# Performance work log

Measured on AMD Instinct MI355X. Metric: run time of the kernel, lower is better.

## Reference

```python
import jax, jax.numpy as jnp
import numpy as np

B, LC, LR, D, H = 32, 2048, 512, 256, 128  # D = 2*hidden_size, fc maps 4*D -> H


def setup_inputs() -> dict:
    key = jax.random.key(0)
    k1, k2, k3, k4 = jax.random.split(key, 4)
    scale = 1.0 / np.sqrt(D)
    return {
        "context_input": jax.random.normal(k1, (B, LC, D), dtype=jnp.float32),
        "response_input": jax.random.normal(k2, (B, LR, D), dtype=jnp.float32),
        "W1": jax.random.normal(k3, (H, 4 * D), dtype=jnp.float32) * scale,
        "b1": jnp.zeros((H,), dtype=jnp.float32),
        "W2": jax.random.normal(k4, (H, 4 * D), dtype=jnp.float32) * scale,
        "b2": jnp.zeros((H,), dtype=jnp.float32),
    }


def reference(context_input, response_input, W1, b1, W2, b2):
    cs = context_input   # [B, Lc, D]
    rs = response_input  # [B, Lr, D]
    # shared score matrix, reused by both softmaxes
    e = jnp.einsum("bcd,brd->bcr", cs, rs)          # [B, Lc, Lr]
    alpha = jax.nn.softmax(e, axis=2)                 # over response positions
    beta = jax.nn.softmax(e, axis=1)                  # over context positions
    cd = jnp.einsum("bcr,brd->bcd", alpha, rs)       # [B, Lc, D]
    rd = jnp.einsum("bcr,bcd->brd", beta, cs)        # [B, Lr, D]
    raw_cl = jnp.concatenate((cs, cd, cs - cd, cs * cd), axis=2)  # [B, Lc, 4D]
    raw_rl = jnp.concatenate((rs, rd, rs - rd, rs * rd), axis=2)  # [B, Lr, 4D]
    # dropout is identity in eval mode
    cl = jax.nn.relu(jnp.einsum("bcf,hf->bch", raw_cl, W1) + b1)  # [B, Lc, H]
    rl = jax.nn.relu(jnp.einsum("brf,hf->brh", raw_rl, W2) + b2)  # [B, Lr, H]
    return (cl, rl)
```

## Files before the change

kernel.cpp:

```cpp
#include <hip/hip_runtime.h>


#define NB  32
#define NLC 2048
#define NLR 512
#define ND  256
#define NH  128

typedef float f32x4 __attribute__((ext_vector_type(4)));
typedef short s16x8 __attribute__((ext_vector_type(8)));
typedef short s16x4 __attribute__((ext_vector_type(4)));

#define WS_CSH 0ull
#define WS_CSL (WS_CSH + 33554432ull)
#define WS_RSH (WS_CSL + 33554432ull)
#define WS_RSL (WS_RSH + 8388608ull)
#define WS_RST (WS_RSL + 8388608ull)
#define WS_CST (WS_RST + 8388608ull)
#define WS_WH  (WS_CST + 33554432ull)
#define WS_NEED (WS_WH + 524288ull)

#define BUFSZ 49152
#define SM_P  98304
#define SM_O  0

__device__ __forceinline__ unsigned short f2bf(float x){
  unsigned u = __builtin_bit_cast(unsigned, x);
  u += 0x7FFFu + ((u >> 16) & 1u);
  return (unsigned short)(u >> 16);
}
__device__ __forceinline__ float bf2f(unsigned short h){
  unsigned u = ((unsigned)h) << 16;
  return __builtin_bit_cast(float, u);
}
__device__ __forceinline__ void splitbf(float x, short &hi, short &lo){
  unsigned short h = f2bf(x);
  float r = x - bf2f(h);
  hi = (short)h;
  lo = (short)f2bf(r);
}
__device__ __forceinline__ void gll16(const void* g, void* l){
  __builtin_amdgcn_global_load_lds((const __attribute__((address_space(1))) void*)g,
                                   (__attribute__((address_space(3))) void*)l, 16, 0, 0);
}


__global__ __launch_bounds__(256)
void prep_rows(const float* __restrict__ cs, const float* __restrict__ rs,
               const float* __restrict__ W1, const float* __restrict__ W2,
               unsigned char* __restrict__ ws)
{
  const int tid = threadIdx.x, lane = tid & 63, wid = tid >> 6;
  const int bid = blockIdx.x;
  if (bid < 20480){
    const float* srcrow; unsigned char *dsth, *dstl; int kvl;
    if (bid < 16384){
      int row = bid*4 + wid;
      int b = row >> 11, pos = row & 2047, t = pos >> 5; kvl = pos & 31;
      srcrow = cs + (size_t)row*ND;
      size_t off = ((size_t)(b*64 + t)*32 + kvl)*512;
      dsth = ws + WS_CSH + off; dstl = ws + WS_CSL + off;
    } else {
      int row = (bid - 16384)*4 + wid;
      int b = row >> 9, pos = row & 511, t = pos >> 5; kvl = pos & 31;
      srcrow = rs + (size_t)row*ND;
      size_t off = ((size_t)(b*16 + t)*32 + kvl)*512;
      dsth = ws + WS_RSH + off; dstl = ws + WS_RSL + off;
    }
    float4 x = *((const float4*)srcrow + lane);
    short h0,l0,h1,l1,h2,l2,h3,l3;
    splitbf(x.x,h0,l0); splitbf(x.y,h1,l1); splitbf(x.z,h2,l2); splitbf(x.w,h3,l3);
    int boff = (8*lane) ^ ((kvl & 7) << 4);
    *(s16x4*)(dsth + boff) = (s16x4){h0,h1,h2,h3};
    *(s16x4*)(dstl + boff) = (s16x4){l0,l1,l2,l3};
  } else {
    int idx = (bid - 20480)*2048 + tid*8;
    const float* srcw = (idx < 131072) ? (W1 + idx) : (W2 + (idx - 131072));
    float4 a = *(const float4*)srcw;
    float4 c4 = *((const float4*)srcw + 1);
    s16x8 h;
    h[0]=(short)f2bf(a.x); h[1]=(short)f2bf(a.y); h[2]=(short)f2bf(a.z); h[3]=(short)f2bf(a.w);
    h[4]=(short)f2bf(c4.x); h[5]=(short)f2bf(c4.y); h[6]=(short)f2bf(c4.z); h[7]=(short)f2bf(c4.w);
    *(s16x8*)(ws + WS_WH + (size_t)idx*2) = h;
  }
}

__global__ __launch_bounds__(256)
void prep_T(const float* __restrict__ cs, const float* __restrict__ rs,
            unsigned char* __restrict__ ws)
{
  __shared__ float tile[32][256];
  const int tid = threadIdx.x, lane = tid & 63, wid = tid >> 6;
  const int bid = blockIdx.x;
  const float* src; unsigned char* dst;
  if (bid < 512){ int b = bid >> 4, t = bid & 15;
    src = rs + ((size_t)b*NLR + t*32)*ND;
    dst = ws + WS_RST + (size_t)bid*16384;
  } else { int b2 = bid - 512; int b = b2 >> 6, t = b2 & 63;
    src = cs + ((size_t)b*NLC + t*32)*ND;
    dst = ws + WS_CST + (size_t)b2*16384;
  }
  #pragma unroll
  for (int i = 0; i < 8; ++i){
    int r = wid*8 + i;
    float4 x = *((const float4*)(src + (size_t)r*ND) + lane);
    *(float4*)&tile[r][lane*4] = x;
  }
  __syncthreads();
  const int d = tid;
  const int swzc = (d >> 2) & 3;
  unsigned char* orow = dst + d*64;
  #pragma unroll
  for (int ci = 0; ci < 4; ++ci){
    int sg = ci ^ swzc;
    s16x8 w;
    #pragma unroll
    for (int j = 0; j < 8; ++j){
      int kvl = 4*sg + (j >> 1) + ((j & 1) << 4);
      w[j] = (short)f2bf(tile[kvl][d]);
    }
    *(s16x8*)(orow + 16*ci) = w;
  }
}


__global__ __launch_bounds__(512, 2)
void lm_main(const unsigned char* __restrict__ ws,
             const float* __restrict__ b1, const float* __restrict__ b2,
             float* __restrict__ out)
{
  __shared__ __align__(16) char smem[106496];

  const int tid  = threadIdx.x;
  const int lane = tid & 63;
  const int wid  = tid >> 6;
  const int c    = lane & 15;
  const int g    = lane >> 4;

  int bid = blockIdx.x;
  int dir, b, qt;
  if (bid < 128){ dir = 1; int xcd = bid & 7, inner = bid >> 3;
    b = xcd*4 + (inner >> 2); qt = inner & 3; }
  else { dir = 0; int t2 = bid - 128; int xcd = t2 & 7, inner = t2 >> 3;
    b = xcd*4 + (inner >> 4); qt = inner & 15; }

  const unsigned char *QH, *QL, *KH, *KL, *VT;
  int NT;
  if (dir == 0){
    QH = ws + WS_CSH + (size_t)b*64*16384;  QL = ws + WS_CSL + (size_t)b*64*16384;
    KH = ws + WS_RSH + (size_t)b*16*16384;  KL = ws + WS_RSL + (size_t)b*16*16384;
    VT = ws + WS_RST + (size_t)b*16*16384;  NT = 16;
  } else {
    QH = ws + WS_RSH + (size_t)b*16*16384;  QL = ws + WS_RSL + (size_t)b*16*16384;
    KH = ws + WS_CSH + (size_t)b*64*16384;  KL = ws + WS_CSL + (size_t)b*64*16384;
    VT = ws + WS_CST + (size_t)b*64*16384;  NT = 64;
  }
  const unsigned char* Wp = ws + WS_WH + (size_t)dir*262144;
  const float* bia = dir ? b2 : b1;
  float* outp = dir == 0 ? out + ((size_t)b*NLC + qt*128)*NH
                         : out + (size_t)NB*NLC*NH + ((size_t)b*NLR + qt*128)*NH;

  s16x8 qh[8], ql[8];
  {
    int q = qt*128 + 16*wid + c;
    const unsigned char* qrowH = QH + (size_t)(q >> 5)*16384 + (size_t)(q & 31)*512;
    const unsigned char* qrowL = QL + (size_t)(q >> 5)*16384 + (size_t)(q & 31)*512;
    int qx = (q & 7) << 4;
    #pragma unroll
    for (int ks = 0; ks < 8; ++ks){
      int off = (64*ks + 16*g) ^ qx;
      qh[ks] = *(const s16x8*)(qrowH + off);
      ql[ks] = *(const s16x8*)(qrowL + off);
    }
  }

  f32x4 o[16];
  #pragma unroll
  for (int i = 0; i < 16; ++i) o[i] = (f32x4){0.f,0.f,0.f,0.f};
  float m_run[4] = {-INFINITY,-INFINITY,-INFINITY,-INFINITY};
  float l_run[4] = {0.f,0.f,0.f,0.f};

  #define STAGE(tt, bsel) do {                                              \
    const unsigned char* kh_ = KH + (size_t)(tt)*16384;                     \
    const unsigned char* kl_ = KL + (size_t)(tt)*16384;                     \
    const unsigned char* vt_ = VT + (size_t)(tt)*16384;                     \
    char* bb_ = smem + (bsel)*BUFSZ;                                        \
    _Pragma("unroll")                                                       \
    for (int i_ = 0; i_ < 6; ++i_){                                         \
      int j_ = 8*i_ + wid;                                                  \
      const unsigned char* src_; int dst_;                                  \
      if (j_ < 16){ src_ = kh_ + (size_t)j_*1024;        dst_ = j_*1024; }  \
      else if (j_ < 32){ src_ = kl_ + (size_t)(j_-16)*1024; dst_ = 16384 + (j_-16)*1024; } \
      else { src_ = vt_ + (size_t)(j_-32)*1024;          dst_ = 32768 + (j_-32)*1024; } \
      gll16(src_ + (size_t)lane*16, bb_ + dst_);                            \
    }                                                                       \
  } while(0)

  STAGE(0, 0);
  __syncthreads();
  int cur = 0;

  for (int t = 0; t < NT; ++t){
    if (t + 1 < NT) STAGE(t + 1, cur ^ 1);

    const char* B = smem + cur*BUFSZ;

    f32x4 s0 = (f32x4){0.f,0.f,0.f,0.f}, s1 = (f32x4){0.f,0.f,0.f,0.f};
    __builtin_amdgcn_s_setprio(1);
    #pragma unroll
    for (int ks = 0; ks < 8; ++ks){
      int kb = 64*ks + 16*g;
      int o0 = c*512 + (kb ^ ((c & 7) << 4));
      int o1 = (16 + c)*512 + (kb ^ (((16 + c) & 7) << 4));
      s16x8 bh0 = *(const s16x8*)(B + o0);
      s16x8 bl0 = *(const s16x8*)(B + 16384 + o0);
      s16x8 bh1 = *(const s16x8*)(B + o1);
      s16x8 bl1 = *(const s16x8*)(B + 16384 + o1);
      s0 = __builtin_amdgcn_mfma_f32_16x16x32_bf16(qh[ks], bh0, s0, 0,0,0);
      s1 = __builtin_amdgcn_mfma_f32_16x16x32_bf16(qh[ks], bh1, s1, 0,0,0);
      s0 = __builtin_amdgcn_mfma_f32_16x16x32_bf16(ql[ks], bh0, s0, 0,0,0);
      s1 = __builtin_amdgcn_mfma_f32_16x16x32_bf16(ql[ks], bh1, s1, 0,0,0);
      s0 = __builtin_amdgcn_mfma_f32_16x16x32_bf16(qh[ks], bl0, s0, 0,0,0);
      s1 = __builtin_amdgcn_mfma_f32_16x16x32_bf16(qh[ks], bl1, s1, 0,0,0);
    }
    __builtin_amdgcn_s_setprio(0);

    float scl[4];
    #pragma unroll
    for (int r = 0; r < 4; ++r){
      float v = fmaxf(s0[r], s1[r]);
      v = fmaxf(v, __shfl_xor(v, 1)); v = fmaxf(v, __shfl_xor(v, 2));
      v = fmaxf(v, __shfl_xor(v, 4)); v = fmaxf(v, __shfl_xor(v, 8));
      float mo = m_run[r];
      float mn = fmaxf(mo, v);
      m_run[r] = mn;
      float sc = __expf(mo - mn);
      scl[r] = sc;
      float p0 = __expf(s0[r] - mn);
      float p1 = __expf(s1[r] - mn);
      float ps = p0 + p1;
      ps += __shfl_xor(ps, 1); ps += __shfl_xor(ps, 2);
      ps += __shfl_xor(ps, 4); ps += __shfl_xor(ps, 8);
      l_run[r] = l_run[r]*sc + ps;
      int qr = 16*wid + 4*g + r;
      unsigned pk = (unsigned)f2bf(p0) | ((unsigned)f2bf(p1) << 16);
      *(unsigned*)(smem + SM_P + qr*64 + ((4*c) ^ (r << 4))) = pk;
    }
    #pragma unroll
    for (int dt = 0; dt < 16; ++dt){
      o[dt][0] *= scl[0]; o[dt][1] *= scl[1]; o[dt][2] *= scl[2]; o[dt][3] *= scl[3];
    }

    {
      int q2 = 16*wid + c;
      s16x8 pa = *(const s16x8*)(smem + SM_P + q2*64 + ((16*g) ^ ((q2 & 3) << 4)));
      __builtin_amdgcn_s_setprio(1);
      #pragma unroll
      for (int dt = 0; dt < 16; ++dt){
        int vrow = 16*dt + c;
        s16x8 vb = *(const s16x8*)(B + 32768 + vrow*64 + ((16*g) ^ (((vrow >> 2) & 3) << 4)));
        o[dt] = __builtin_amdgcn_mfma_f32_16x16x32_bf16(pa, vb, o[dt], 0,0,0);
      }
      __builtin_amdgcn_s_setprio(0);
    }

    __syncthreads();
    cur ^= 1;
  }

  {
    float inv[4];
    #pragma unroll
    for (int r = 0; r < 4; ++r) inv[r] = 1.0f / l_run[r];
    #pragma unroll
    for (int dt = 0; dt < 16; ++dt){
      #pragma unroll
      for (int r = 0; r < 4; ++r){
        int qr = 16*wid + 4*g + r;
        int dcol = 16*dt + c;
        float val = o[dt][r] * inv[r];
        *(short*)(smem + SM_O + qr*512 + ((2*dcol) ^ ((qr & 7) << 4))) = (short)f2bf(val);
      }
    }
  }

  f32x4 fa[8];
  #pragma unroll
  for (int i = 0; i < 8; ++i) fa[i] = (f32x4){0.f,0.f,0.f,0.f};

  #pragma unroll
  for (int fc = 0; fc < 8; ++fc){
    #pragma unroll
    for (int ksl = 0; ksl < 4; ++ksl){
      const int cidx = (fc & 1)*4 + ksl;
      s16x8 a;
      if (fc < 2){
        a = qh[cidx];
      } else {
        int q2 = 16*wid + c;
        s16x8 o8 = *(const s16x8*)(smem + SM_O + q2*512 + ((64*cidx + 16*g) ^ ((q2 & 7) << 4)));
        if (fc < 4){ a = o8; }
        else {
          #pragma unroll
          for (int j = 0; j < 8; ++j){
            float qf = bf2f((unsigned short)qh[cidx][j]) + bf2f((unsigned short)ql[cidx][j]);
            float of = bf2f((unsigned short)o8[j]);
            float fv = (fc < 6) ? (qf - of) : (qf * of);
            a[j] = (short)f2bf(fv);
          }
        }
      }
      #pragma unroll
      for (int nt = 0; nt < 8; ++nt){
        s16x8 wb = *(const s16x8*)(Wp + (size_t)(16*nt + c)*2048 + 2*(fc*128 + 32*ksl + 8*g));
        fa[nt] = __builtin_amdgcn_mfma_f32_16x16x32_bf16(a, wb, fa[nt], 0,0,0);
      }
    }
  }

  #pragma unroll
  for (int nt = 0; nt < 8; ++nt){
    float bs = bia[16*nt + c];
    #pragma unroll
    for (int r = 0; r < 4; ++r){
      int qr = 16*wid + 4*g + r;
      float v = fa[nt][r] + bs;
      v = fmaxf(v, 0.f);
      outp[(size_t)qr*NH + 16*nt + c] = v;
    }
  }
}


__global__ __launch_bounds__(256, 2)
void lm_fallback(const float* __restrict__ cs, const float* __restrict__ rs,
                 const float* __restrict__ W1, const float* __restrict__ b1,
                 const float* __restrict__ W2, const float* __restrict__ b2,
                 float* __restrict__ out)
{
  __shared__ __align__(16) char smem[65536];
  const int tid  = threadIdx.x;
  const int lane = tid & 63;
  const int wid  = tid >> 6;
  const int c    = lane & 15;
  const int g    = lane >> 4;

  int bid = blockIdx.x;
  int dir, b, qt;
  if (bid < 1024){ int xcd = bid & 7, inner = bid >> 3;
    b = (xcd << 2) + (inner >> 5); qt = inner & 31; dir = 0; }
  else { int t2 = bid - 1024; int xcd = t2 & 7, inner = t2 >> 3;
    b = (xcd << 2) + (inner >> 3); qt = inner & 7; dir = 1; }

  const float* Q   = dir == 0 ? cs + ((size_t)b*NLC + qt*64)*ND
                              : rs + ((size_t)b*NLR + qt*64)*ND;
  const float* KV  = dir == 0 ? rs + (size_t)b*NLR*ND : cs + (size_t)b*NLC*ND;
  const int    NK  = dir == 0 ? NLR : NLC;
  const float* Wm  = dir == 0 ? W1 : W2;
  const float* bia = dir == 0 ? b1 : b2;
  float* outp = dir == 0 ? out + ((size_t)b*NLC + qt*64)*NH
                         : out + (size_t)NB*NLC*NH + ((size_t)b*NLR + qt*64)*NH;

  s16x8 qh[8], ql[8];
  {
    const float* qrow = Q + (size_t)(16*wid + c)*ND;
    #pragma unroll
    for (int ks = 0; ks < 8; ++ks){
      float4 x0 = *(const float4*)(qrow + 32*ks + 8*g);
      float4 x1 = *(const float4*)(qrow + 32*ks + 8*g + 4);
      float xs[8] = {x0.x,x0.y,x0.z,x0.w,x1.x,x1.y,x1.z,x1.w};
      #pragma unroll
      for (int j = 0; j < 8; ++j){ short h,l; splitbf(xs[j],h,l); qh[ks][j]=h; ql[ks][j]=l; }
    }
  }

  f32x4 o[16];
  #pragma unroll
  for (int i = 0; i < 16; ++i) o[i] = (f32x4){0.f,0.f,0.f,0.f};
  float m_run[4] = {-INFINITY,-INFINITY,-INFINITY,-INFINITY};
  float l_run[4] = {0.f,0.f,0.f,0.f};

  const int ntile = NK >> 5;
  for (int t = 0; t < ntile; ++t){
    __syncthreads();
    {
      const float* KVt = KV + (size_t)t*32*ND;
      #pragma unroll
      for (int p = 0; p < 8; ++p){
        int kvloc = p*4 + wid;
        float4 x = *((const float4*)(KVt + kvloc*ND) + lane);
        short h0,l0,h1,l1,h2,l2,h3,l3;
        splitbf(x.x,h0,l0); splitbf(x.y,h1,l1); splitbf(x.z,h2,l2); splitbf(x.w,h3,l3);
        int roff = kvloc*512 + ((8*lane) ^ ((kvloc&7)<<4));
        *(s16x4*)(smem + 0     + roff) = (s16x4){h0,h1,h2,h3};
        *(s16x4*)(smem + 16384 + roff) = (s16x4){l0,l1,l2,l3};
        int d0 = 4*lane;
        short hs[4] = {h0,h1,h2,h3};
        #pragma unroll
        for (int j = 0; j < 4; ++j){
          int dr = d0 + j;
          int voff = dr*64 + ((2*kvloc) ^ (((dr>>2)&3)<<4));
          *(short*)(smem + 32768 + voff) = hs[j];
        }
      }
    }
    __syncthreads();

    f32x4 s0 = (f32x4){0.f,0.f,0.f,0.f}, s1 = (f32x4){0.f,0.f,0.f,0.f};
    #pragma unroll
    for (int ks = 0; ks < 8; ++ks){
      int kb = 64*ks + 16*g;
      int o0 = c*512 + (kb ^ ((c&7)<<4));
      int o1 = (16+c)*512 + (kb ^ (((16+c)&7)<<4));
      s16x8 bh0 = *(const s16x8*)(smem + 0     + o0);
      s16x8 bl0 = *(const s16x8*)(smem + 16384 + o0);
      s16x8 bh1 = *(const s16x8*)(smem + 0     + o1);
      s16x8 bl1 = *(const s16x8*)(smem + 16384 + o1);
      s0 = __builtin_amdgcn_mfma_f32_16x16x32_bf16(qh[ks], bh0, s0, 0,0,0);
      s1 = __builtin_amdgcn_mfma_f32_16x16x32_bf16(qh[ks], bh1, s1, 0,0,0);
      s0 = __builtin_amdgcn_mfma_f32_16x16x32_bf16(ql[ks], bh0, s0, 0,0,0);
      s1 = __builtin_amdgcn_mfma_f32_16x16x32_bf16(ql[ks], bh1, s1, 0,0,0);
      s0 = __builtin_amdgcn_mfma_f32_16x16x32_bf16(qh[ks], bl0, s0, 0,0,0);
      s1 = __builtin_amdgcn_mfma_f32_16x16x32_bf16(qh[ks], bl1, s1, 0,0,0);
    }

    float scl[4];
    #pragma unroll
    for (int r = 0; r < 4; ++r){
      float v = fmaxf(s0[r], s1[r]);
      v = fmaxf(v, __shfl_xor(v, 1)); v = fmaxf(v, __shfl_xor(v, 2));
      v = fmaxf(v, __shfl_xor(v, 4)); v = fmaxf(v, __shfl_xor(v, 8));
      float mo = m_run[r];
      float mn = fmaxf(mo, v);
      m_run[r] = mn;
      float sc = __expf(mo - mn);
      scl[r] = sc;
      float p0 = __expf(s0[r] - mn);
      float p1 = __expf(s1[r] - mn);
      float ps = p0 + p1;
      ps += __shfl_xor(ps, 1); ps += __shfl_xor(ps, 2);
      ps += __shfl_xor(ps, 4); ps += __shfl_xor(ps, 8);
      l_run[r] = l_run[r]*sc + ps;
      int q = 16*wid + 4*g + r;
      int pb = q*64;
      *(short*)(smem + 49152 + pb + (( 2*c     ) ^ (r<<4))) = (short)f2bf(p0);
      *(short*)(smem + 49152 + pb + ((32 + 2*c ) ^ (r<<4))) = (short)f2bf(p1);
    }
    #pragma unroll
    for (int dt = 0; dt < 16; ++dt){
      o[dt][0] *= scl[0]; o[dt][1] *= scl[1]; o[dt][2] *= scl[2]; o[dt][3] *= scl[3];
    }

    {
      int q = 16*wid + c;
      s16x8 pa = *(const s16x8*)(smem + 49152 + q*64 + ((16*g) ^ ((q&3)<<4)));
      #pragma unroll
      for (int dt = 0; dt < 16; ++dt){
        int vrow = 16*dt + c;
        s16x8 vb = *(const s16x8*)(smem + 32768 + vrow*64 + ((16*g) ^ (((vrow>>2)&3)<<4)));
        o[dt] = __builtin_amdgcn_mfma_f32_16x16x32_bf16(pa, vb, o[dt], 0,0,0);
      }
    }
  }

  __syncthreads();
  {
    float inv[4];
    #pragma unroll
    for (int r = 0; r < 4; ++r) inv[r] = 1.0f / l_run[r];
    #pragma unroll
    for (int dt = 0; dt < 16; ++dt){
      #pragma unroll
      for (int r = 0; r < 4; ++r){
        int q = 16*wid + 4*g + r;
        int dcol = 16*dt + c;
        float val = o[dt][r] * inv[r];
        *(short*)(smem + 0 + q*512 + ((2*dcol) ^ ((q&7)<<4))) = (short)f2bf(val);
      }
    }
  }

  f32x4 fa[8];
  #pragma unroll
  for (int i = 0; i < 8; ++i) fa[i] = (f32x4){0.f,0.f,0.f,0.f};

  #pragma unroll
  for (int fc = 0; fc < 8; ++fc){
    __syncthreads();
    #pragma unroll
    for (int p = 0; p < 8; ++p){
      int h  = p*16 + (tid >> 4);
      int fl = (tid & 15) * 8;
      const float* srcw = Wm + (size_t)h*1024 + fc*128 + fl;
      float4 x0 = *(const float4*)srcw;
      float4 x1 = *(const float4*)(srcw + 4);
      s16x8 w8;
      w8[0]=(short)f2bf(x0.x); w8[1]=(short)f2bf(x0.y); w8[2]=(short)f2bf(x0.z); w8[3]=(short)f2bf(x0.w);
      w8[4]=(short)f2bf(x1.x); w8[5]=(short)f2bf(x1.y); w8[6]=(short)f2bf(x1.z); w8[7]=(short)f2bf(x1.w);
      *(s16x8*)(smem + 32768 + h*256 + ((2*fl) ^ ((h&7)<<4))) = w8;
    }
    __syncthreads();
    #pragma unroll
    for (int ks = 0; ks < 4; ++ks){
      const int cidx = (fc & 1)*4 + ks;
      s16x8 a;
      if (fc < 2){
        a = qh[cidx];
      } else {
        int q = 16*wid + c;
        s16x8 o8 = *(const s16x8*)(smem + 0 + q*512 + ((64*cidx + 16*g) ^ ((q&7)<<4)));
        if (fc < 4){ a = o8; }
        else {
          #pragma unroll
          for (int j = 0; j < 8; ++j){
            float qf = bf2f((unsigned short)qh[cidx][j]) + bf2f((unsigned short)ql[cidx][j]);
            float of = bf2f((unsigned short)o8[j]);
            float fv = (fc < 6) ? (qf - of) : (qf * of);
            a[j] = (short)f2bf(fv);
          }
        }
      }
      #pragma unroll
      for (int nt = 0; nt < 8; ++nt){
        int hh = 16*nt + c;
        s16x8 wb = *(const s16x8*)(smem + 32768 + hh*256 + ((64*ks + 16*g) ^ ((hh&7)<<4)));
        fa[nt] = __builtin_amdgcn_mfma_f32_16x16x32_bf16(a, wb, fa[nt], 0,0,0);
      }
    }
  }

  #pragma unroll
  for (int nt = 0; nt < 8; ++nt){
    float bs = bia[16*nt + c];
    #pragma unroll
    for (int r = 0; r < 4; ++r){
      int q = 16*wid + 4*g + r;
      float v = fa[nt][r] + bs;
      v = fmaxf(v, 0.f);
      outp[(size_t)q*NH + 16*nt + c] = v;
    }
  }
}

extern "C" void kernel_launch(void* const* d_in, const int* in_sizes, int n_in,
                              void* d_out, int out_size, void* d_ws, size_t ws_size,
                              hipStream_t stream) {
  (void)in_sizes; (void)n_in; (void)out_size;
  const float* cs = (const float*)d_in[0];
  const float* rs = (const float*)d_in[1];
  const float* W1 = (const float*)d_in[2];
  const float* b1 = (const float*)d_in[3];
  const float* W2 = (const float*)d_in[4];
  const float* b2 = (const float*)d_in[5];
  float* out = (float*)d_out;

  if (ws_size >= WS_NEED){
    unsigned char* ws = (unsigned char*)d_ws;
    hipLaunchKernelGGL(prep_rows, dim3(20608), dim3(256), 0, stream, cs, rs, W1, W2, ws);
    hipLaunchKernelGGL(prep_T,    dim3(2560),  dim3(256), 0, stream, cs, rs, ws);
    hipLaunchKernelGGL(lm_main,   dim3(640),   dim3(512), 0, stream, ws, b1, b2, out);
  } else {
    hipLaunchKernelGGL(lm_fallback, dim3(1280), dim3(256), 0, stream,
                       cs, rs, W1, b1, W2, b2, out);
  }
}
```

Before: 484.3 us.

## Transpose score MFMA so softmax stays in registers, dropping P staging through LDS

Swaps the MFMA operand order so each lane holds one query's scores across key positions. The row max and sum now need only two cross-lane shuffles, and the probability fragment is packed directly into the B operand of the PV MFMA instead of round-tripping through shared memory. The V-transpose pack order is changed to match the new operand layout. Score accumulation is split into two interleaved accumulators to shorten MFMA dependency chains. This shrinks LDS use, adds one barrier before the epilogue, and relies on the reworked layout being consistent across the prep and main kernels.

```diff
diff --git a/kernel.cpp b/kernel.cpp
--- a/kernel.cpp
+++ b/kernel.cpp
@@ -10,6 +10,7 @@
 typedef float f32x4 __attribute__((ext_vector_type(4)));
 typedef short s16x8 __attribute__((ext_vector_type(8)));
 typedef short s16x4 __attribute__((ext_vector_type(4)));
+typedef int   i32x4 __attribute__((ext_vector_type(4)));
 
 #define WS_CSH 0ull
 #define WS_CSL (WS_CSH + 33554432ull)
@@ -21,7 +22,6 @@
 #define WS_NEED (WS_WH + 524288ull)
 
 #define BUFSZ 49152
-#define SM_P  98304
 #define SM_O  0
 
 __device__ __forceinline__ unsigned short f2bf(float x){
@@ -116,7 +116,7 @@
     s16x8 w;
     #pragma unroll
     for (int j = 0; j < 8; ++j){
-      int kvl = 4*sg + (j >> 1) + ((j & 1) << 4);
+      int kvl = 4*sg + (j & 3) + 16*((j >> 2) & 1);
       w[j] = (short)f2bf(tile[kvl][d]);
     }
     *(s16x8*)(orow + 16*ci) = w;
@@ -129,7 +129,7 @@
              const float* __restrict__ b1, const float* __restrict__ b2,
              float* __restrict__ out)
 {
-  __shared__ __align__(16) char smem[106496];
+  __shared__ __align__(16) char smem[98304];
 
   const int tid  = threadIdx.x;
   const int lane = tid & 63;
@@ -177,8 +177,8 @@
   f32x4 o[16];
   #pragma unroll
   for (int i = 0; i < 16; ++i) o[i] = (f32x4){0.f,0.f,0.f,0.f};
-  float m_run[4] = {-INFINITY,-INFINITY,-INFINITY,-INFINITY};
-  float l_run[4] = {0.f,0.f,0.f,0.f};
+  float m_run = -INFINITY;
+  float l_run = 0.f;
 
   #define STAGE(tt, bsel) do {                                              \
     const unsigned char* kh_ = KH + (size_t)(tt)*16384;                     \
@@ -205,7 +205,8 @@
 
     const char* B = smem + cur*BUFSZ;
 
-    f32x4 s0 = (f32x4){0.f,0.f,0.f,0.f}, s1 = (f32x4){0.f,0.f,0.f,0.f};
+    f32x4 s0a = (f32x4){0.f,0.f,0.f,0.f}, s0b = (f32x4){0.f,0.f,0.f,0.f};
+    f32x4 s1a = (f32x4){0.f,0.f,0.f,0.f}, s1b = (f32x4){0.f,0.f,0.f,0.f};
     __builtin_amdgcn_s_setprio(1);
     #pragma unroll
     for (int ks = 0; ks < 8; ++ks){
@@ -216,73 +217,79 @@
       s16x8 bl0 = *(const s16x8*)(B + 16384 + o0);
       s16x8 bh1 = *(const s16x8*)(B + o1);
       s16x8 bl1 = *(const s16x8*)(B + 16384 + o1);
-      s0 = __builtin_amdgcn_mfma_f32_16x16x32_bf16(qh[ks], bh0, s0, 0,0,0);
-      s1 = __builtin_amdgcn_mfma_f32_16x16x32_bf16(qh[ks], bh1, s1, 0,0,0);
-      s0 = __builtin_amdgcn_mfma_f32_16x16x32_bf16(ql[ks], bh0, s0, 0,0,0);
-      s1 = __builtin_amdgcn_mfma_f32_16x16x32_bf16(ql[ks], bh1, s1, 0,0,0);
-      s0 = __builtin_amdgcn_mfma_f32_16x16x32_bf16(qh[ks], bl0, s0, 0,0,0);
-      s1 = __builtin_amdgcn_mfma_f32_16x16x32_bf16(qh[ks], bl1, s1, 0,0,0);
+      if (ks & 1){
+        s0b = __builtin_amdgcn_mfma_f32_16x16x32_bf16(bh0, qh[ks], s0b, 0,0,0);
+        s1b = __builtin_amdgcn_mfma_f32_16x16x32_bf16(bh1, qh[ks], s1b, 0,0,0);
+        s0b = __builtin_amdgcn_mfma_f32_16x16x32_bf16(bh0, ql[ks], s0b, 0,0,0);
+        s1b = __builtin_amdgcn_mfma_f32_16x16x32_bf16(bh1, ql[ks], s1b, 0,0,0);
+        s0b = __builtin_amdgcn_mfma_f32_16x16x32_bf16(bl0, qh[ks], s0b, 0,0,0);
+        s1b = __builtin_amdgcn_mfma_f32_16x16x32_bf16(bl1, qh[ks], s1b, 0,0,0);
+      } else {
+        s0a = __builtin_amdgcn_mfma_f32_16x16x32_bf16(bh0, qh[ks], s0a, 0,0,0);
+        s1a = __builtin_amdgcn_mfma_f32_16x16x32_bf16(bh1, qh[ks], s1a, 0,0,0);
+        s0a = __builtin_amdgcn_mfma_f32_16x16x32_bf16(bh0, ql[ks], s0a, 0,0,0);
+        s1a = __builtin_amdgcn_mfma_f32_16x16x32_bf16(bh1, ql[ks], s1a, 0,0,0);
+        s0a = __builtin_amdgcn_mfma_f32_16x16x32_bf16(bl0, qh[ks], s0a, 0,0,0);
+        s1a = __builtin_amdgcn_mfma_f32_16x16x32_bf16(bl1, qh[ks], s1a, 0,0,0);
+      }
     }
     __builtin_amdgcn_s_setprio(0);
-
-    float scl[4];
-    #pragma unroll
-    for (int r = 0; r < 4; ++r){
-      float v = fmaxf(s0[r], s1[r]);
-      v = fmaxf(v, __shfl_xor(v, 1)); v = fmaxf(v, __shfl_xor(v, 2));
-      v = fmaxf(v, __shfl_xor(v, 4)); v = fmaxf(v, __shfl_xor(v, 8));
-      float mo = m_run[r];
-      float mn = fmaxf(mo, v);
-      m_run[r] = mn;
-      float sc = __expf(mo - mn);
-      scl[r] = sc;
-      float p0 = __expf(s0[r] - mn);
-      float p1 = __expf(s1[r] - mn);
-      float ps = p0 + p1;
-      ps += __shfl_xor(ps, 1); ps += __shfl_xor(ps, 2);
-      ps += __shfl_xor(ps, 4); ps += __shfl_xor(ps, 8);
-      l_run[r] = l_run[r]*sc + ps;
-      int qr = 16*wid + 4*g + r;
-      unsigned pk = (unsigned)f2bf(p0) | ((unsigned)f2bf(p1) << 16);
-      *(unsigned*)(smem + SM_P + qr*64 + ((4*c) ^ (r << 4))) = pk;
-    }
-    #pragma unroll
-    for (int dt = 0; dt < 16; ++dt){
-      o[dt][0] *= scl[0]; o[dt][1] *= scl[1]; o[dt][2] *= scl[2]; o[dt][3] *= scl[3];
-    }
-
-    {
-      int q2 = 16*wid + c;
-      s16x8 pa = *(const s16x8*)(smem + SM_P + q2*64 + ((16*g) ^ ((q2 & 3) << 4)));
-      __builtin_amdgcn_s_setprio(1);
-      #pragma unroll
-      for (int dt = 0; dt < 16; ++dt){
-        int vrow = 16*dt + c;
-        s16x8 vb = *(const s16x8*)(B + 32768 + vrow*64 + ((16*g) ^ (((vrow >> 2) & 3) << 4)));
-        o[dt] = __builtin_amdgcn_mfma_f32_16x16x32_bf16(pa, vb, o[dt], 0,0,0);
-      }
-      __builtin_amdgcn_s_setprio(0);
-    }
+    f32x4 s0 = s0a + s0b;
+    f32x4 s1 = s1a + s1b;
+
+    float v = fmaxf(fmaxf(fmaxf(s0[0], s0[1]), fmaxf(s0[2], s0[3])),
+                    fmaxf(fmaxf(s1[0], s1[1]), fmaxf(s1[2], s1[3])));
+    v = fmaxf(v, __shfl_xor(v, 16));
+    v = fmaxf(v, __shfl_xor(v, 32));
+    float mn  = fmaxf(m_run, v);
+    float scl = __expf(m_run - mn);
+    m_run = mn;
+    float p0_0 = __expf(s0[0] - mn), p0_1 = __expf(s0[1] - mn);
+    float p0_2 = __expf(s0[2] - mn), p0_3 = __expf(s0[3] - mn);
+    float p1_0 = __expf(s1[0] - mn), p1_1 = __expf(s1[1] - mn);
+    float p1_2 = __expf(s1[2] - mn), p1_3 = __expf(s1[3] - mn);
+    float ps = ((p0_0 + p0_1) + (p0_2 + p0_3)) + ((p1_0 + p1_1) + (p1_2 + p1_3));
+    ps += __shfl_xor(ps, 16);
+    ps += __shfl_xor(ps, 32);
+    l_run = l_run * scl + ps;
+
+    unsigned pw0 = (unsigned)f2bf(p0_0) | ((unsigned)f2bf(p0_1) << 16);
+    unsigned pw1 = (unsigned)f2bf(p0_2) | ((unsigned)f2bf(p0_3) << 16);
+    unsigned pw2 = (unsigned)f2bf(p1_0) | ((unsigned)f2bf(p1_1) << 16);
+    unsigned pw3 = (unsigned)f2bf(p1_2) | ((unsigned)f2bf(p1_3) << 16);
+    s16x8 pb = __builtin_bit_cast(s16x8, (i32x4){(int)pw0, (int)pw1, (int)pw2, (int)pw3});
+
+    #pragma unroll
+    for (int m = 0; m < 16; ++m){
+      o[m][0] *= scl; o[m][1] *= scl; o[m][2] *= scl; o[m][3] *= scl;
+    }
+
+    __builtin_amdgcn_s_setprio(1);
+    #pragma unroll
+    for (int m = 0; m < 16; ++m){
+      int vrow = 16*m + c;
+      s16x8 va = *(const s16x8*)(B + 32768 + vrow*64 + ((16*g) ^ (((vrow >> 2) & 3) << 4)));
+      o[m] = __builtin_amdgcn_mfma_f32_16x16x32_bf16(va, pb, o[m], 0,0,0);
+    }
+    __builtin_amdgcn_s_setprio(0);
 
     __syncthreads();
     cur ^= 1;
   }
 
   {
-    float inv[4];
-    #pragma unroll
-    for (int r = 0; r < 4; ++r) inv[r] = 1.0f / l_run[r];
-    #pragma unroll
-    for (int dt = 0; dt < 16; ++dt){
-      #pragma unroll
-      for (int r = 0; r < 4; ++r){
-        int qr = 16*wid + 4*g + r;
-        int dcol = 16*dt + c;
-        float val = o[dt][r] * inv[r];
-        *(short*)(smem + SM_O + qr*512 + ((2*dcol) ^ ((qr & 7) << 4))) = (short)f2bf(val);
-      }
-    }
-  }
+    float inv = 1.0f / l_run;
+    int q = 16*wid + c;
+    int swz = (q & 7) << 4;
+    #pragma unroll
+    for (int m = 0; m < 16; ++m){
+      unsigned u0 = (unsigned)f2bf(o[m][0]*inv) | ((unsigned)f2bf(o[m][1]*inv) << 16);
+      unsigned u1 = (unsigned)f2bf(o[m][2]*inv) | ((unsigned)f2bf(o[m][3]*inv) << 16);
+      int byte = q*512 + ((32*m + 8*g) ^ swz);
+      *(uint2*)(smem + SM_O + byte) = (uint2){u0, u1};
+    }
+  }
+  __syncthreads();
 
   f32x4 fa[8];
   #pragma unroll
@@ -324,9 +331,9 @@
     #pragma unroll
     for (int r = 0; r < 4; ++r){
       int qr = 16*wid + 4*g + r;
-      float v = fa[nt][r] + bs;
-      v = fmaxf(v, 0.f);
-      outp[(size_t)qr*NH + 16*nt + c] = v;
+      float v2 = fa[nt][r] + bs;
+      v2 = fmaxf(v2, 0.f);
+      outp[(size_t)qr*NH + 16*nt + c] = v2;
     }
   }
 }
```

After: 443.6 us. -8.4%, faster.
